# Kernel optimization log

Hardware: AMD Instinct MI355X
Metric: run time of the kernel (lower is better)

## Reference

```python
import jax, jax.numpy as jnp
import numpy as np

LAMBDA = 0.95   # fast-weight decay
ETA = 0.5       # Hebbian write rate
EPS = 1e-5      # LayerNorm epsilon
S_LOOP = 2      # inner read steps


def setup_inputs() -> dict:
    key = jax.random.key(0)
    ks = jax.random.split(key, 3)
    T, B, d_g, d_h = 32, 32, 256, 512
    z_seq = jax.random.normal(ks[0], (T, B, d_g), dtype=jnp.float32)
    # kaiming-uniform-ish / xavier-ish scaled weights
    W_h = jax.random.normal(ks[1], (d_h, d_h), dtype=jnp.float32) * (2.0 / d_h) ** 0.5
    W_g = jax.random.normal(ks[2], (d_h, d_g), dtype=jnp.float32) * (2.0 / (d_h + d_g)) ** 0.5
    b_h = jnp.zeros((d_h,), jnp.float32)
    ln_gamma = jnp.ones((d_h,), jnp.float32)
    ln_beta = jnp.zeros((d_h,), jnp.float32)
    return {"z_seq": z_seq, "W_h": W_h, "W_g": W_g, "b_h": b_h,
            "ln_gamma": ln_gamma, "ln_beta": ln_beta}


def reference(z_seq, W_h, W_g, b_h, ln_gamma, ln_beta):
    T, B, _ = z_seq.shape
    d_h = W_h.shape[0]

    def ln(x):
        mu = jnp.mean(x, axis=-1, keepdims=True)
        var = jnp.mean((x - mu) ** 2, axis=-1, keepdims=True)
        return (x - mu) * jax.lax.rsqrt(var + EPS) * ln_gamma + ln_beta

    def inner_read(h_base, A):
        # h = relu(LN(h_base)); then S fast-weight reads h <- relu(LN(h_base + A h))
        h = jax.nn.relu(ln(h_base))
        for _ in range(S_LOOP):
            Ah = jnp.einsum('bij,bj->bi', A, h)  # [B, d_h]
            h = jax.nn.relu(ln(h_base + Ah))
        return h

    def step(carry, z_t):
        h, A = carry
        h_base = h @ W_h.T + z_t @ W_g.T + b_h  # [B, d_h]
        h = inner_read(h_base, A)
        # Hebbian outer-product write: A <- lambda*A + eta * h h^T
        A = LAMBDA * A + ETA * jnp.einsum('bi,bj->bij', h, h)
        return (h, A), None

    h0 = jnp.zeros((B, d_h), z_seq.dtype)
    A0 = jnp.zeros((B, d_h, d_h), z_seq.dtype)
    (h, A), _ = jax.lax.scan(step, (h0, A0), z_seq[:-1])

    # last step: read-only (no A update)
    h_base = h @ W_h.T + z_seq[-1] @ W_g.T + b_h
    h = inner_read(h_base, A)
    return h
```

## Files before the change

### kernel.cpp

```cpp
#include <hip/hip_runtime.h>

typedef __attribute__((ext_vector_type(8))) short short8;
typedef __attribute__((ext_vector_type(4))) float f32x4;

constexpr int T_STEPS = 32;
constexpr int BATCH   = 32;
constexpr int DG      = 256;
constexpr int DH      = 512;
constexpr int NHIST   = 31;
constexpr int LDA     = 544;
constexpr int LDT     = 40;
constexpr float LAMBDA_ = 0.95f;
constexpr float ETA_    = 0.5f;
constexpr float EPS_    = 1e-5f;

__device__ __forceinline__ uint bf16cvt(float f) {
  uint u = __float_as_uint(f);
  return (u + 0x7FFFu + ((u >> 16) & 1u)) >> 16;
}
__device__ __forceinline__ uint pack2(float a, float b) {
  return bf16cvt(a) | (bf16cvt(b) << 16);
}

__global__ __launch_bounds__(512) void pack_kernel(
    const float* __restrict__ Wh, uint4* __restrict__ Wp) {
  const int f  = blockIdx.x * 512 + threadIdx.x;
  const int lf = f & 63;
  const int kk = (f >> 6) & 15;
  const int mt = f >> 10;
  const int r  = mt * 16 + (lf & 15);
  const int k0 = kk * 32 + (lf >> 4) * 8;
  const float4 a = *reinterpret_cast<const float4*>(Wh + (size_t)r * DH + k0);
  const float4 b = *reinterpret_cast<const float4*>(Wh + (size_t)r * DH + k0 + 4);
  Wp[f] = make_uint4(pack2(a.x, a.y), pack2(a.z, a.w),
                     pack2(b.x, b.y), pack2(b.z, b.w));
}

__global__ __launch_bounds__(512, 2)
__attribute__((amdgpu_waves_per_eu(2, 2)))
void rnn_kernel(
    const uint4* __restrict__ Wp, const float* __restrict__ z,
    const float* __restrict__ Wg, const float* __restrict__ bh,
    const float* __restrict__ g, const float* __restrict__ be,
    float* __restrict__ out) {
  __shared__ float  area[T_STEPS * LDA];
  __shared__ ushort histT[DH][LDT];
  __shared__ float  part[DH];
  __shared__ float  h_s[DH];
  __shared__ ushort hbf[DH];
  __shared__ float  red1[8], red2[8];
  __shared__ float  cc[NHIST + 1];
  __shared__ float  lam_pow[NHIST];

  const int tid  = threadIdx.x;
  const int lane = tid & 63;
  const int wave = tid >> 6;
  const int c    = lane & 15;
  const int gq   = lane >> 4;
  const int b    = blockIdx.x;
  const int r    = tid;

  if (tid == 0) {
    float p = 1.f;
    for (int k = 0; k < NHIST; ++k) { lam_pow[k] = p; p *= LAMBDA_; }
  }
  if (tid < NHIST + 1) cc[tid] = 0.f;
  {
    uint4 zz = make_uint4(0u, 0u, 0u, 0u);
#pragma unroll
    for (int i = 0; i < 5; ++i)
      reinterpret_cast<uint4*>(&histT[r][0])[i] = zz;
  }

  uint4 wfr[4][8];
#pragma unroll
  for (int mt4 = 0; mt4 < 4; ++mt4)
#pragma unroll
    for (int kk = 0; kk < 8; ++kk)
      wfr[mt4][kk] = Wp[(size_t)((wave * 4 + mt4) * 16 + kk) * 64 + lane];

#pragma unroll
  for (int mt4 = 0; mt4 < 4; ++mt4) {
    const int mt = wave * 4 + mt4;
    f32x4 acc0 = {0.f,0.f,0.f,0.f}, acc1 = {0.f,0.f,0.f,0.f};
#pragma unroll
    for (int kk = 0; kk < 8; ++kk) {
      const int k0 = kk * 32 + gq * 8;
      const float4 a  = *reinterpret_cast<const float4*>(Wg + (size_t)(mt*16 + c) * DG + k0);
      const float4 a2 = *reinterpret_cast<const float4*>(Wg + (size_t)(mt*16 + c) * DG + k0 + 4);
      const uint4 afu = make_uint4(pack2(a.x,a.y), pack2(a.z,a.w),
                                   pack2(a2.x,a2.y), pack2(a2.z,a2.w));
      const float* zb0 = z + ((size_t)c        * BATCH + b) * DG + k0;
      const float* zb1 = z + ((size_t)(16 + c) * BATCH + b) * DG + k0;
      const float4 b00 = *reinterpret_cast<const float4*>(zb0);
      const float4 b01 = *reinterpret_cast<const float4*>(zb0 + 4);
      const float4 b10 = *reinterpret_cast<const float4*>(zb1);
      const float4 b11 = *reinterpret_cast<const float4*>(zb1 + 4);
      const uint4 bf0 = make_uint4(pack2(b00.x,b00.y), pack2(b00.z,b00.w),
                                   pack2(b01.x,b01.y), pack2(b01.z,b01.w));
      const uint4 bf1 = make_uint4(pack2(b10.x,b10.y), pack2(b10.z,b10.w),
                                   pack2(b11.x,b11.y), pack2(b11.z,b11.w));
      acc0 = __builtin_amdgcn_mfma_f32_16x16x32_bf16(
          __builtin_bit_cast(short8, afu), __builtin_bit_cast(short8, bf0), acc0, 0,0,0);
      acc1 = __builtin_amdgcn_mfma_f32_16x16x32_bf16(
          __builtin_bit_cast(short8, afu), __builtin_bit_cast(short8, bf1), acc1, 0,0,0);
    }
    *reinterpret_cast<f32x4*>(&area[(size_t)c        * LDA + mt*16 + gq*4]) = acc0;
    *reinterpret_cast<f32x4*>(&area[(size_t)(16 + c) * LDA + mt*16 + gq*4]) = acc1;
  }
  __syncthreads();

  const float bh_r = bh[r], g_r = g[r], be_r = be[r];

  auto ln = [&](float x) -> float {
    float s1 = x, s2 = x * x;
#pragma unroll
    for (int off = 32; off; off >>= 1) {
      s1 += __shfl_xor(s1, off, 64);
      s2 += __shfl_xor(s2, off, 64);
    }
    if (lane == 0) { red1[wave] = s1; red2[wave] = s2; }
    __syncthreads();
    float a = 0.f, q = 0.f;
#pragma unroll
    for (int w2 = 0; w2 < 8; ++w2) { a += red1[w2]; q += red2[w2]; }
    const float mu = a * (1.f / DH);
    const float rs = rsqrtf(q * (1.f / DH) - mu * mu + EPS_);
    const float hv2 = fmaxf((x - mu) * rs * g_r + be_r, 0.f);
    h_s[r] = hv2;
    hbf[r] = (ushort)bf16cvt(hv2);
    __syncthreads();
    return hv2;
  };

  float hv = 0.f;
  for (int t = 0; t < T_STEPS; ++t) {
    float xb;
    if (t == 0) {
      xb = area[r] + bh_r;
    } else {
      f32x4 acc[4] = {{0.f,0.f,0.f,0.f},{0.f,0.f,0.f,0.f},
                      {0.f,0.f,0.f,0.f},{0.f,0.f,0.f,0.f}};
#pragma unroll
      for (int kk = 0; kk < 8; ++kk) {
        uint4 bvu = {0u,0u,0u,0u};
        if (c == 0)
          bvu = *reinterpret_cast<const uint4*>(&hbf[kk*32 + gq*8]);
        const short8 bv = __builtin_bit_cast(short8, bvu);
#pragma unroll
        for (int mt4 = 0; mt4 < 4; ++mt4)
          acc[mt4] = __builtin_amdgcn_mfma_f32_16x16x32_bf16(
              __builtin_bit_cast(short8, wfr[mt4][kk]), bv, acc[mt4], 0,0,0);
      }
#pragma unroll
      for (int kk = 8; kk < 16; ++kk) {
        uint4 bvu = {0u,0u,0u,0u};
        if (c == 0)
          bvu = *reinterpret_cast<const uint4*>(&hbf[kk*32 + gq*8]);
        const short8 bv = __builtin_bit_cast(short8, bvu);
#pragma unroll
        for (int mt4 = 0; mt4 < 4; ++mt4) {
          const uint4 au = Wp[(size_t)((wave*4 + mt4)*16 + kk) * 64 + lane];
          acc[mt4] = __builtin_amdgcn_mfma_f32_16x16x32_bf16(
              __builtin_bit_cast(short8, au), bv, acc[mt4], 0,0,0);
        }
      }
      if (c == 0) {
#pragma unroll
        for (int mt4 = 0; mt4 < 4; ++mt4)
          *reinterpret_cast<f32x4*>(&part[(wave*4 + mt4)*16 + gq*4]) = acc[mt4];
      }
      __syncthreads();
      xb = part[r] + area[(size_t)t * LDA + r] + bh_r;
    }

    hv = ln(xb);

    if (t > 0) {
      for (int s = 0; s < 2; ++s) {
        const float4 c0 = *reinterpret_cast<const float4*>(&h_s[lane * 8]);
        const float4 c1 = *reinterpret_cast<const float4*>(&h_s[lane * 8 + 4]);
        for (int sp = wave; sp < t; sp += 8) {
          const float* hr = &area[(size_t)sp * LDA];
          const float4 a0 = *reinterpret_cast<const float4*>(&hr[lane * 8]);
          const float4 a1 = *reinterpret_cast<const float4*>(&hr[lane * 8 + 4]);
          float d = c0.x*a0.x + c0.y*a0.y + c0.z*a0.z + c0.w*a0.w
                  + c1.x*a1.x + c1.y*a1.y + c1.z*a1.z + c1.w*a1.w;
#pragma unroll
          for (int off = 32; off; off >>= 1) d += __shfl_xor(d, off, 64);
          if (lane == 0) cc[sp] = ETA_ * lam_pow[t - 1 - sp] * d;
        }
        __syncthreads();
        float ah = 0.f;
#pragma unroll
        for (int q8 = 0; q8 < 4; ++q8) {
          const uint4 hw = *reinterpret_cast<const uint4*>(&histT[r][q8 * 8]);
          const uint w0 = hw.x, w1 = hw.y, w2 = hw.z, w3 = hw.w;
          ah = fmaf(cc[q8*8+0], __uint_as_float(w0 << 16),          ah);
          ah = fmaf(cc[q8*8+1], __uint_as_float(w0 & 0xFFFF0000u),  ah);
          ah = fmaf(cc[q8*8+2], __uint_as_float(w1 << 16),          ah);
          ah = fmaf(cc[q8*8+3], __uint_as_float(w1 & 0xFFFF0000u),  ah);
          ah = fmaf(cc[q8*8+4], __uint_as_float(w2 << 16),          ah);
          ah = fmaf(cc[q8*8+5], __uint_as_float(w2 & 0xFFFF0000u),  ah);
          ah = fmaf(cc[q8*8+6], __uint_as_float(w3 << 16),          ah);
          ah = fmaf(cc[q8*8+7], __uint_as_float(w3 & 0xFFFF0000u),  ah);
        }
        hv = ln(xb + ah);
      }
    }

    if (t < T_STEPS - 1) {
      area[(size_t)t * LDA + r] = hv;
      histT[r][t] = (ushort)bf16cvt(hv);
    }
  }

  out[(size_t)b * DH + r] = hv;
}

extern "C" void kernel_launch(void* const* d_in, const int* in_sizes, int n_in,
                              void* d_out, int out_size, void* d_ws, size_t ws_size,
                              hipStream_t stream) {
  const float* z     = (const float*)d_in[0];
  const float* W_h   = (const float*)d_in[1];
  const float* W_g   = (const float*)d_in[2];
  const float* b_h   = (const float*)d_in[3];
  const float* gamma = (const float*)d_in[4];
  const float* beta  = (const float*)d_in[5];
  float* out = (float*)d_out;

  uint4* Wp = (uint4*)d_ws;

  pack_kernel<<<dim3(64), dim3(512), 0, stream>>>(W_h, Wp);
  rnn_kernel<<<dim3(BATCH), dim3(512), 0, stream>>>(Wp, z, W_g, b_h,
                                                    gamma, beta, out);
}
```

Before: 292.3 us.

## Stream W_h fragments through LDS with async loads and spill z projection to global

Drops the 32 register-resident W_h fragments and instead streams all 16 k-slices per step through a double-buffered LDS staging area using global_load_lds, with explicit vmcnt waits. The precomputed z@W_g^T projection moves from shared memory to a global workspace, and the history used for the dot products is stored as bf16 instead of fp32. The aim is to free registers and LDS and to overlap weight loads with MFMA work. In exchange every step reloads all weights from global or L2 and inserts wait barriers, and the history dot products lose precision.

```diff
diff --git a/kernel.cpp b/kernel.cpp
--- a/kernel.cpp
+++ b/kernel.cpp
@@ -8,7 +8,7 @@
 constexpr int DG      = 256;
 constexpr int DH      = 512;
 constexpr int NHIST   = 31;
-constexpr int LDA     = 544;
+constexpr int LDH     = 520;
 constexpr int LDT     = 40;
 constexpr float LAMBDA_ = 0.95f;
 constexpr float ETA_    = 0.5f;
@@ -36,14 +36,13 @@
                      pack2(b.x, b.y), pack2(b.z, b.w));
 }
 
-__global__ __launch_bounds__(512, 2)
-__attribute__((amdgpu_waves_per_eu(2, 2)))
-void rnn_kernel(
+__global__ __launch_bounds__(512, 2) void rnn_kernel(
     const uint4* __restrict__ Wp, const float* __restrict__ z,
     const float* __restrict__ Wg, const float* __restrict__ bh,
     const float* __restrict__ g, const float* __restrict__ be,
-    float* __restrict__ out) {
-  __shared__ float  area[T_STEPS * LDA];
+    float* __restrict__ ZGg, float* __restrict__ out) {
+  __shared__ uint4  stage[8][2][4][64];
+  __shared__ ushort hist_bf[NHIST][LDH];
   __shared__ ushort histT[DH][LDT];
   __shared__ float  part[DH];
   __shared__ float  h_s[DH];
@@ -72,12 +71,16 @@
       reinterpret_cast<uint4*>(&histT[r][0])[i] = zz;
   }
 
-  uint4 wfr[4][8];
-#pragma unroll
-  for (int mt4 = 0; mt4 < 4; ++mt4)
-#pragma unroll
-    for (int kk = 0; kk < 8; ++kk)
-      wfr[mt4][kk] = Wp[(size_t)((wave * 4 + mt4) * 16 + kk) * 64 + lane];
+  auto STAGE = [&](int kk, int slot) {
+#pragma unroll
+    for (int mt4 = 0; mt4 < 4; ++mt4) {
+      const uint4* gsrc = Wp + (size_t)((wave * 4 + mt4) * 16 + kk) * 64 + lane;
+      __builtin_amdgcn_global_load_lds(
+          (const __attribute__((address_space(1))) uint*)gsrc,
+          (__attribute__((address_space(3))) uint*)&stage[wave][slot][mt4][0],
+          16, 0, 0);
+    }
+  };
 
 #pragma unroll
   for (int mt4 = 0; mt4 < 4; ++mt4) {
@@ -105,8 +108,8 @@
       acc1 = __builtin_amdgcn_mfma_f32_16x16x32_bf16(
           __builtin_bit_cast(short8, afu), __builtin_bit_cast(short8, bf1), acc1, 0,0,0);
     }
-    *reinterpret_cast<f32x4*>(&area[(size_t)c        * LDA + mt*16 + gq*4]) = acc0;
-    *reinterpret_cast<f32x4*>(&area[(size_t)(16 + c) * LDA + mt*16 + gq*4]) = acc1;
+    *reinterpret_cast<f32x4*>(&ZGg[((size_t)c        * BATCH + b) * DH + mt*16 + gq*4]) = acc0;
+    *reinterpret_cast<f32x4*>(&ZGg[((size_t)(16 + c) * BATCH + b) * DH + mt*16 + gq*4]) = acc1;
   }
   __syncthreads();
 
@@ -137,33 +140,39 @@
   for (int t = 0; t < T_STEPS; ++t) {
     float xb;
     if (t == 0) {
-      xb = area[r] + bh_r;
+      xb = ZGg[(size_t)b * DH + r] + bh_r;
     } else {
+      const float zgv = ZGg[((size_t)t * BATCH + b) * DH + r];
+      asm volatile("s_waitcnt vmcnt(0)" ::: "memory");
+      __builtin_amdgcn_sched_barrier(0);
+
+      STAGE(0, 0);
+      STAGE(1, 1);
       f32x4 acc[4] = {{0.f,0.f,0.f,0.f},{0.f,0.f,0.f,0.f},
                       {0.f,0.f,0.f,0.f},{0.f,0.f,0.f,0.f}};
 #pragma unroll
-      for (int kk = 0; kk < 8; ++kk) {
+      for (int kk = 0; kk < 16; ++kk) {
+        const int slot = kk & 1;
+        if (kk < 15) { asm volatile("s_waitcnt vmcnt(4)" ::: "memory"); }
+        else         { asm volatile("s_waitcnt vmcnt(0)" ::: "memory"); }
+        __builtin_amdgcn_sched_barrier(0);
+        const uint4 a0 = stage[wave][slot][0][lane];
+        const uint4 a1 = stage[wave][slot][1][lane];
+        const uint4 a2 = stage[wave][slot][2][lane];
+        const uint4 a3 = stage[wave][slot][3][lane];
         uint4 bvu = {0u,0u,0u,0u};
         if (c == 0)
           bvu = *reinterpret_cast<const uint4*>(&hbf[kk*32 + gq*8]);
         const short8 bv = __builtin_bit_cast(short8, bvu);
-#pragma unroll
-        for (int mt4 = 0; mt4 < 4; ++mt4)
-          acc[mt4] = __builtin_amdgcn_mfma_f32_16x16x32_bf16(
-              __builtin_bit_cast(short8, wfr[mt4][kk]), bv, acc[mt4], 0,0,0);
-      }
-#pragma unroll
-      for (int kk = 8; kk < 16; ++kk) {
-        uint4 bvu = {0u,0u,0u,0u};
-        if (c == 0)
-          bvu = *reinterpret_cast<const uint4*>(&hbf[kk*32 + gq*8]);
-        const short8 bv = __builtin_bit_cast(short8, bvu);
-#pragma unroll
-        for (int mt4 = 0; mt4 < 4; ++mt4) {
-          const uint4 au = Wp[(size_t)((wave*4 + mt4)*16 + kk) * 64 + lane];
-          acc[mt4] = __builtin_amdgcn_mfma_f32_16x16x32_bf16(
-              __builtin_bit_cast(short8, au), bv, acc[mt4], 0,0,0);
-        }
+        acc[0] = __builtin_amdgcn_mfma_f32_16x16x32_bf16(
+            __builtin_bit_cast(short8, a0), bv, acc[0], 0,0,0);
+        acc[1] = __builtin_amdgcn_mfma_f32_16x16x32_bf16(
+            __builtin_bit_cast(short8, a1), bv, acc[1], 0,0,0);
+        acc[2] = __builtin_amdgcn_mfma_f32_16x16x32_bf16(
+            __builtin_bit_cast(short8, a2), bv, acc[2], 0,0,0);
+        acc[3] = __builtin_amdgcn_mfma_f32_16x16x32_bf16(
+            __builtin_bit_cast(short8, a3), bv, acc[3], 0,0,0);
+        if (kk < 14) STAGE(kk + 2, slot);
       }
       if (c == 0) {
 #pragma unroll
@@ -171,7 +180,7 @@
           *reinterpret_cast<f32x4*>(&part[(wave*4 + mt4)*16 + gq*4]) = acc[mt4];
       }
       __syncthreads();
-      xb = part[r] + area[(size_t)t * LDA + r] + bh_r;
+      xb = part[r] + zgv + bh_r;
     }
 
     hv = ln(xb);
@@ -181,11 +190,16 @@
         const float4 c0 = *reinterpret_cast<const float4*>(&h_s[lane * 8]);
         const float4 c1 = *reinterpret_cast<const float4*>(&h_s[lane * 8 + 4]);
         for (int sp = wave; sp < t; sp += 8) {
-          const float* hr = &area[(size_t)sp * LDA];
-          const float4 a0 = *reinterpret_cast<const float4*>(&hr[lane * 8]);
-          const float4 a1 = *reinterpret_cast<const float4*>(&hr[lane * 8 + 4]);
-          float d = c0.x*a0.x + c0.y*a0.y + c0.z*a0.z + c0.w*a0.w
-                  + c1.x*a1.x + c1.y*a1.y + c1.z*a1.z + c1.w*a1.w;
+          const uint4 hw = *reinterpret_cast<const uint4*>(&hist_bf[sp][lane * 8]);
+          float d;
+          d =      __uint_as_float(hw.x << 16)          * c0.x;
+          d = fmaf(__uint_as_float(hw.x & 0xFFFF0000u), c0.y, d);
+          d = fmaf(__uint_as_float(hw.y << 16),         c0.z, d);
+          d = fmaf(__uint_as_float(hw.y & 0xFFFF0000u), c0.w, d);
+          d = fmaf(__uint_as_float(hw.z << 16),         c1.x, d);
+          d = fmaf(__uint_as_float(hw.z & 0xFFFF0000u), c1.y, d);
+          d = fmaf(__uint_as_float(hw.w << 16),         c1.z, d);
+          d = fmaf(__uint_as_float(hw.w & 0xFFFF0000u), c1.w, d);
 #pragma unroll
           for (int off = 32; off; off >>= 1) d += __shfl_xor(d, off, 64);
           if (lane == 0) cc[sp] = ETA_ * lam_pow[t - 1 - sp] * d;
@@ -210,8 +224,9 @@
     }
 
     if (t < T_STEPS - 1) {
-      area[(size_t)t * LDA + r] = hv;
-      histT[r][t] = (ushort)bf16cvt(hv);
+      const ushort hb16 = (ushort)bf16cvt(hv);
+      hist_bf[t][r] = hb16;
+      histT[r][t]   = hb16;
     }
   }
 
@@ -229,9 +244,10 @@
   const float* beta  = (const float*)d_in[5];
   float* out = (float*)d_out;
 
-  uint4* Wp = (uint4*)d_ws;
+  float* ZGg = (float*)d_ws;
+  uint4* Wp  = (uint4*)((char*)d_ws + (size_t)T_STEPS * BATCH * DH * 4);
 
   pack_kernel<<<dim3(64), dim3(512), 0, stream>>>(W_h, Wp);
   rnn_kernel<<<dim3(BATCH), dim3(512), 0, stream>>>(Wp, z, W_g, b_h,
-                                                    gamma, beta, out);
-}
+                                                    gamma, beta, ZGg, out);
+}
```

Result: slower. 307.9 us (+5.3%).
